# Kernel optimization log

Hardware: AMD Instinct MI355X
Metric: run time of the kernel (lower is better)

Reference implementation:

```python
import jax, jax.numpy as jnp
import numpy as np

TOP_K = 32
SCALE_FACTOR = 8.0
NEG_INF = -1e18


def setup_inputs() -> dict:
    key = jax.random.key(0)
    kq, kk, kv = jax.random.split(key, 3)
    B, H, S, D = 2, 16, 2048, 64
    q = jax.random.normal(kq, (B, H, S, D), dtype=jnp.float32)
    k = jax.random.normal(kk, (B, H, S, D), dtype=jnp.float32)
    v = jax.random.normal(kv, (B, H, S, D), dtype=jnp.float32)
    return {"q": q, "k": k, "v": v}


def reference(q, k, v):
    # scores: [B, H, Sq, Sk]
    scores = jnp.einsum("bhqd,bhkd->bhqk", q, k) / SCALE_FACTOR
    # torch code clamps top_k against key.size()[-1] == head dim D (quirk);
    # with TOP_K=32 < D=64 the clamp is inactive.
    top_k = min(TOP_K, k.shape[-1])
    topv, _ = jax.lax.top_k(scores, top_k)            # [B,H,Sq,top_k], sorted desc
    thresh = topv[..., -1:]                            # k-th largest per query row
    mask_k = scores < thresh                           # True -> masked out
    scores = jnp.where(mask_k, NEG_INF, scores)
    attn = jax.nn.softmax(scores, axis=-1)
    context = jnp.einsum("bhqk,bhkd->bhqd", attn, v)
    return context, attn, mask_k
```

## Files before the change

### kernel.cpp

```cpp
#include <hip/hip_runtime.h>
#include <math.h>

namespace {
constexpr int kS = 2048;
constexpr int kD = 64;
constexpr int kBH = 32;
constexpr int kTopK = 32;
constexpr int kBins = 4096;
constexpr int kMaxCand = 256;
constexpr int kKeepCap = 64;
constexpr size_t kCtxElems  = (size_t)kBH * kS * kD;
constexpr size_t kAttnElems = (size_t)kBH * kS * kS;
}

__device__ __forceinline__ unsigned sortable_bits(float x) {
  unsigned u = __float_as_uint(x);
  return u ^ ((u & 0x80000000u) ? 0xFFFFFFFFu : 0x80000000u);
}

__global__ __launch_bounds__(256) void qk_scores(const float* __restrict__ q,
                                                 const float* __restrict__ k,
                                                 float* __restrict__ scores) {
  __shared__ float QsT[64][132];
  __shared__ float KsT[64][132];
  const int bh  = blockIdx.z;
  const int q0  = blockIdx.y * 128;
  const int k0  = blockIdx.x * 128;
  const int tid = threadIdx.x;
  const float* qg = q + ((size_t)bh * kS + q0) * kD;
  const float* kg = k + ((size_t)bh * kS + k0) * kD;

#pragma unroll
  for (int rnd = 0; rnd < 8; ++rnd) {
    int flat = rnd * 1024 + tid * 4;
    int r = flat >> 6;
    int c = flat & 63;
    float4 qv = *(const float4*)(qg + flat);
    QsT[c + 0][r] = qv.x;
    QsT[c + 1][r] = qv.y;
    QsT[c + 2][r] = qv.z;
    QsT[c + 3][r] = qv.w;
    float4 kv = *(const float4*)(kg + flat);
    KsT[c + 0][r] = kv.x;
    KsT[c + 1][r] = kv.y;
    KsT[c + 2][r] = kv.z;
    KsT[c + 3][r] = kv.w;
  }
  __syncthreads();

  const int ty8 = (tid >> 4) * 8;
  const int tx8 = (tid & 15) * 8;
  float acc[8][8] = {};
#pragma unroll
  for (int kk = 0; kk < 64; kk += 4) {
    float a[4][8], b[4][8];
#pragma unroll
    for (int u = 0; u < 4; ++u) {
      *(float4*)(&a[u][0]) = *(const float4*)(&QsT[kk + u][ty8]);
      *(float4*)(&a[u][4]) = *(const float4*)(&QsT[kk + u][ty8 + 4]);
      *(float4*)(&b[u][0]) = *(const float4*)(&KsT[kk + u][tx8]);
      *(float4*)(&b[u][4]) = *(const float4*)(&KsT[kk + u][tx8 + 4]);
    }
#pragma unroll
    for (int i = 0; i < 8; ++i)
#pragma unroll
      for (int u = 0; u < 4; ++u)
#pragma unroll
        for (int j = 0; j < 8; ++j)
          acc[i][j] += a[u][i] * b[u][j];
  }

#pragma unroll
  for (int i = 0; i < 8; ++i) {
    float* orow = scores + ((size_t)bh * kS + q0 + ty8 + i) * kS + k0 + tx8;
    float4 o0 = make_float4(acc[i][0] * 0.125f, acc[i][1] * 0.125f,
                            acc[i][2] * 0.125f, acc[i][3] * 0.125f);
    float4 o1 = make_float4(acc[i][4] * 0.125f, acc[i][5] * 0.125f,
                            acc[i][6] * 0.125f, acc[i][7] * 0.125f);
    *(float4*)(orow)     = o0;
    *(float4*)(orow + 4) = o1;
  }
}

__global__ __launch_bounds__(256) void topk_softmax(const float* __restrict__ v,
                                                    float* __restrict__ ctx,
                                                    float* __restrict__ attn,
                                                    float* __restrict__ mask) {
  const int row  = blockIdx.x;
  const int bh   = row >> 11;
  const int tid  = threadIdx.x;
  const int lane = tid & 63;
  const int wid  = tid >> 6;

  __shared__ unsigned s_hist[kBins];
  __shared__ float    s_cand[kMaxCand];
  __shared__ int      s_kidx[kKeepCap];
  __shared__ float    s_kw[kKeepCap];
  __shared__ float    s_wmax[4], s_wsum[4];
  __shared__ unsigned s_T[4];
  __shared__ unsigned s_nc, s_nk;
  __shared__ int      s_bstar, s_gabove;
  __shared__ float    s_t32;

  const float* srow = attn + (size_t)row * kS;
  float4 l0 = *(const float4*)(srow + tid * 4);
  float4 l1 = *(const float4*)(srow + 1024 + tid * 4);
  float locv[8] = {l0.x, l0.y, l0.z, l0.w, l1.x, l1.y, l1.z, l1.w};
  int   loce[8];
#pragma unroll
  for (int j = 0; j < 8; ++j)
    loce[j] = (j < 4) ? (tid * 4 + j) : (1024 + tid * 4 + (j - 4));
#pragma unroll
  for (int i = 0; i < 4; ++i)
    *(uint4*)(&s_hist[tid * 16 + i * 4]) = make_uint4(0u, 0u, 0u, 0u);
  if (tid == 0) { s_nc = 0u; s_nk = 0u; }
  __syncthreads();

  unsigned bins[8];
  float pmax = locv[0];
#pragma unroll
  for (int j = 0; j < 8; ++j) {
    bins[j] = sortable_bits(locv[j]) >> 20;
    atomicAdd(&s_hist[bins[j]], 1u);
    pmax = fmaxf(pmax, locv[j]);
  }
#pragma unroll
  for (int off = 32; off >= 1; off >>= 1)
    pmax = fmaxf(pmax, __shfl_xor(pmax, off));
  if (lane == 0) s_wmax[wid] = pmax;
  __syncthreads();

  unsigned lsum = 0;
#pragma unroll
  for (int j = 0; j < 16; ++j) lsum += s_hist[tid * 16 + j];
  unsigned sfx = lsum;
#pragma unroll
  for (int off = 1; off < 64; off <<= 1) {
    unsigned z = __shfl_down(sfx, off);
    if (lane + off < 64) sfx += z;
  }
  if (lane == 0) s_T[wid] = sfx;
  __syncthreads();

  unsigned hi = 0;
#pragma unroll
  for (int w = 0; w < 4; ++w)
    if (w > wid) hi += s_T[w];
  unsigned gsfx  = sfx + hi;
  unsigned above = gsfx - lsum;
  if (gsfx >= (unsigned)kTopK && above < (unsigned)kTopK) {
    unsigned run = above;
    for (int j = 15; j >= 0; --j) {
      unsigned h = s_hist[tid * 16 + j];
      if (run < (unsigned)kTopK && run + h >= (unsigned)kTopK) {
        s_bstar  = tid * 16 + j;
        s_gabove = (int)run;
      }
      run += h;
    }
  }
  __syncthreads();
  const int   bstar  = s_bstar;
  const int   gabove = s_gabove;
  const float mx = fmaxf(fmaxf(s_wmax[0], s_wmax[1]),
                         fmaxf(s_wmax[2], s_wmax[3]));

#pragma unroll
  for (int j = 0; j < 8; ++j) {
    if ((int)bins[j] == bstar) {
      unsigned pos = atomicAdd(&s_nc, 1u);
      if (pos < (unsigned)kMaxCand) s_cand[pos] = locv[j];
    }
  }
  __syncthreads();
  const int m2 = (int)min(s_nc, (unsigned)kMaxCand);

  for (int c = tid; c < m2; c += 256) {
    float x = s_cand[c];
    int g = 0, e = 0;
    for (int j2 = 0; j2 < m2; ++j2) {
      float y = s_cand[j2];
      g += (y > x);
      e += (y == x);
    }
    int G = gabove + g;
    if (G < kTopK && G + e >= kTopK) s_t32 = x;
  }
  __syncthreads();
  const float t32 = s_t32;

  float w8[8];
  float psum = 0.0f;
#pragma unroll
  for (int j = 0; j < 8; ++j) {
    bool keep = (locv[j] >= t32);
    float wv = keep ? __expf(locv[j] - mx) : 0.0f;
    w8[j] = wv;
    psum += wv;
    if (keep) {
      unsigned p = atomicAdd(&s_nk, 1u);
      if (p < (unsigned)kKeepCap) { s_kidx[p] = loce[j]; s_kw[p] = wv; }
    }
  }
#pragma unroll
  for (int off = 32; off >= 1; off >>= 1)
    psum += __shfl_xor(psum, off);
  if (lane == 0) s_wsum[wid] = psum;
  __syncthreads();

  const float Z = s_wsum[0] + s_wsum[1] + s_wsum[2] + s_wsum[3];
  const float invZ = 1.0f / Z;

  float* arow = attn + (size_t)row * kS;
  float* mrow = mask + (size_t)row * kS;
  float4 a0 = make_float4(w8[0] * invZ, w8[1] * invZ, w8[2] * invZ, w8[3] * invZ);
  float4 a1 = make_float4(w8[4] * invZ, w8[5] * invZ, w8[6] * invZ, w8[7] * invZ);
  float4 m0 = make_float4(locv[0] >= t32 ? 0.f : 1.f, locv[1] >= t32 ? 0.f : 1.f,
                          locv[2] >= t32 ? 0.f : 1.f, locv[3] >= t32 ? 0.f : 1.f);
  float4 m1 = make_float4(locv[4] >= t32 ? 0.f : 1.f, locv[5] >= t32 ? 0.f : 1.f,
                          locv[6] >= t32 ? 0.f : 1.f, locv[7] >= t32 ? 0.f : 1.f);
  *(float4*)(arow + tid * 4)        = a0;
  *(float4*)(arow + 1024 + tid * 4) = a1;
  *(float4*)(mrow + tid * 4)        = m0;
  *(float4*)(mrow + 1024 + tid * 4) = m1;

  if (tid < kD) {
    const int nk = (int)min(s_nk, (unsigned)kKeepCap);
    float acc = 0.0f;
    for (int c = 0; c < nk; ++c)
      acc += s_kw[c] * v[((size_t)bh * kS + s_kidx[c]) * kD + tid];
    ctx[(size_t)row * kD + tid] = acc * invZ;
  }
}

extern "C" void kernel_launch(void* const* d_in, const int* in_sizes, int n_in,
                              void* d_out, int out_size, void* d_ws, size_t ws_size,
                              hipStream_t stream) {
  const float* q = (const float*)d_in[0];
  const float* k = (const float*)d_in[1];
  const float* v = (const float*)d_in[2];
  float* out  = (float*)d_out;
  float* ctx  = out;
  float* attn = out + kCtxElems;
  float* mask = attn + kAttnElems;

  dim3 g1(kS / 128, kS / 128, kBH);
  qk_scores<<<g1, 256, 0, stream>>>(q, k, attn);
  topk_softmax<<<dim3(kBH * kS), 256, 0, stream>>>(v, ctx, attn, mask);
}
```

Measured before the change: 1.434 ms.

## Process one top-k softmax row per wavefront and split QK staging into halves

```diff
diff --git a/kernel.cpp b/kernel.cpp
--- a/kernel.cpp
+++ b/kernel.cpp
@@ -6,8 +6,8 @@
 constexpr int kD = 64;
 constexpr int kBH = 32;
 constexpr int kTopK = 32;
-constexpr int kBins = 4096;
-constexpr int kMaxCand = 256;
+constexpr int kPadBins = 2112;
+constexpr int kCandCap = 128;
 constexpr int kKeepCap = 64;
 constexpr size_t kCtxElems  = (size_t)kBH * kS * kD;
 constexpr size_t kAttnElems = (size_t)kBH * kS * kS;
@@ -21,8 +21,8 @@
 __global__ __launch_bounds__(256) void qk_scores(const float* __restrict__ q,
                                                  const float* __restrict__ k,
                                                  float* __restrict__ scores) {
-  __shared__ float QsT[64][132];
-  __shared__ float KsT[64][132];
+  __shared__ float QsT[32][132];
+  __shared__ float KsT[32][132];
   const int bh  = blockIdx.z;
   const int q0  = blockIdx.y * 128;
   const int k0  = blockIdx.x * 128;
@@ -30,44 +30,43 @@
   const float* qg = q + ((size_t)bh * kS + q0) * kD;
   const float* kg = k + ((size_t)bh * kS + k0) * kD;
 
-#pragma unroll
-  for (int rnd = 0; rnd < 8; ++rnd) {
-    int flat = rnd * 1024 + tid * 4;
-    int r = flat >> 6;
-    int c = flat & 63;
-    float4 qv = *(const float4*)(qg + flat);
-    QsT[c + 0][r] = qv.x;
-    QsT[c + 1][r] = qv.y;
-    QsT[c + 2][r] = qv.z;
-    QsT[c + 3][r] = qv.w;
-    float4 kv = *(const float4*)(kg + flat);
-    KsT[c + 0][r] = kv.x;
-    KsT[c + 1][r] = kv.y;
-    KsT[c + 2][r] = kv.z;
-    KsT[c + 3][r] = kv.w;
-  }
-  __syncthreads();
-
   const int ty8 = (tid >> 4) * 8;
   const int tx8 = (tid & 15) * 8;
   float acc[8][8] = {};
-#pragma unroll
-  for (int kk = 0; kk < 64; kk += 4) {
-    float a[4][8], b[4][8];
-#pragma unroll
-    for (int u = 0; u < 4; ++u) {
-      *(float4*)(&a[u][0]) = *(const float4*)(&QsT[kk + u][ty8]);
-      *(float4*)(&a[u][4]) = *(const float4*)(&QsT[kk + u][ty8 + 4]);
-      *(float4*)(&b[u][0]) = *(const float4*)(&KsT[kk + u][tx8]);
-      *(float4*)(&b[u][4]) = *(const float4*)(&KsT[kk + u][tx8 + 4]);
-    }
-#pragma unroll
-    for (int i = 0; i < 8; ++i)
-#pragma unroll
-      for (int u = 0; u < 4; ++u)
+
+  for (int half = 0; half < 2; ++half) {
+    if (half) __syncthreads();
+#pragma unroll
+    for (int rnd = 0; rnd < 4; ++rnd) {
+      int flat = rnd * 1024 + tid * 4;
+      int r = flat >> 5;
+      int c = flat & 31;
+      float4 qv = *(const float4*)(qg + r * kD + half * 32 + c);
+      QsT[c + 0][r] = qv.x;
+      QsT[c + 1][r] = qv.y;
+      QsT[c + 2][r] = qv.z;
+      QsT[c + 3][r] = qv.w;
+      float4 kv = *(const float4*)(kg + r * kD + half * 32 + c);
+      KsT[c + 0][r] = kv.x;
+      KsT[c + 1][r] = kv.y;
+      KsT[c + 2][r] = kv.z;
+      KsT[c + 3][r] = kv.w;
+    }
+    __syncthreads();
+
+#pragma unroll
+    for (int kk = 0; kk < 32; ++kk) {
+      float a[8], b[8];
+      *(float4*)(&a[0]) = *(const float4*)(&QsT[kk][ty8]);
+      *(float4*)(&a[4]) = *(const float4*)(&QsT[kk][ty8 + 4]);
+      *(float4*)(&b[0]) = *(const float4*)(&KsT[kk][tx8]);
+      *(float4*)(&b[4]) = *(const float4*)(&KsT[kk][tx8 + 4]);
+#pragma unroll
+      for (int i = 0; i < 8; ++i)
 #pragma unroll
         for (int j = 0; j < 8; ++j)
-          acc[i][j] += a[u][i] * b[u][j];
+          acc[i][j] += a[i] * b[j];
+    }
   }
 
 #pragma unroll
@@ -86,151 +85,153 @@
                                                     float* __restrict__ ctx,
                                                     float* __restrict__ attn,
                                                     float* __restrict__ mask) {
-  const int row  = blockIdx.x;
+  __shared__ unsigned s_hist[4][kPadBins];
+  __shared__ float    s_cand[4][kCandCap];
+  __shared__ int      s_kidx[4][kKeepCap];
+  __shared__ float    s_kw[4][kKeepCap];
+  __shared__ unsigned s_nc[4], s_nk[4];
+
+  const int tid  = threadIdx.x;
+  const int wid  = tid >> 6;
+  const int lane = tid & 63;
+  const int row  = blockIdx.x * 4 + wid;
   const int bh   = row >> 11;
-  const int tid  = threadIdx.x;
-  const int lane = tid & 63;
-  const int wid  = tid >> 6;
-
-  __shared__ unsigned s_hist[kBins];
-  __shared__ float    s_cand[kMaxCand];
-  __shared__ int      s_kidx[kKeepCap];
-  __shared__ float    s_kw[kKeepCap];
-  __shared__ float    s_wmax[4], s_wsum[4];
-  __shared__ unsigned s_T[4];
-  __shared__ unsigned s_nc, s_nk;
-  __shared__ int      s_bstar, s_gabove;
-  __shared__ float    s_t32;
+  unsigned* hist = s_hist[wid];
 
   const float* srow = attn + (size_t)row * kS;
-  float4 l0 = *(const float4*)(srow + tid * 4);
-  float4 l1 = *(const float4*)(srow + 1024 + tid * 4);
-  float locv[8] = {l0.x, l0.y, l0.z, l0.w, l1.x, l1.y, l1.z, l1.w};
-  int   loce[8];
-#pragma unroll
-  for (int j = 0; j < 8; ++j)
-    loce[j] = (j < 4) ? (tid * 4 + j) : (1024 + tid * 4 + (j - 4));
-#pragma unroll
-  for (int i = 0; i < 4; ++i)
-    *(uint4*)(&s_hist[tid * 16 + i * 4]) = make_uint4(0u, 0u, 0u, 0u);
-  if (tid == 0) { s_nc = 0u; s_nk = 0u; }
-  __syncthreads();
-
-  unsigned bins[8];
+  float locv[32];
+#pragma unroll
+  for (int g = 0; g < 8; ++g)
+    *(float4*)(&locv[g * 4]) = *(const float4*)(srow + g * 256 + lane * 4);
+
+#pragma unroll
+  for (int j = 0; j < 33; ++j) hist[j * 64 + lane] = 0u;
+  if (lane == 0) { s_nc[wid] = 0u; s_nk[wid] = 0u; }
+
   float pmax = locv[0];
 #pragma unroll
-  for (int j = 0; j < 8; ++j) {
-    bins[j] = sortable_bits(locv[j]) >> 20;
-    atomicAdd(&s_hist[bins[j]], 1u);
+  for (int j = 0; j < 32; ++j) {
+    unsigned b = sortable_bits(locv[j]) >> 21;
+    atomicAdd(&hist[b + (b >> 5)], 1u);
     pmax = fmaxf(pmax, locv[j]);
   }
 #pragma unroll
   for (int off = 32; off >= 1; off >>= 1)
     pmax = fmaxf(pmax, __shfl_xor(pmax, off));
-  if (lane == 0) s_wmax[wid] = pmax;
-  __syncthreads();
+
+  asm volatile("s_waitcnt lgkmcnt(0)" ::: "memory");
 
   unsigned lsum = 0;
 #pragma unroll
-  for (int j = 0; j < 16; ++j) lsum += s_hist[tid * 16 + j];
+  for (int j = 0; j < 32; ++j) lsum += hist[lane * 33 + j];
   unsigned sfx = lsum;
 #pragma unroll
   for (int off = 1; off < 64; off <<= 1) {
     unsigned z = __shfl_down(sfx, off);
     if (lane + off < 64) sfx += z;
   }
-  if (lane == 0) s_T[wid] = sfx;
-  __syncthreads();
-
-  unsigned hi = 0;
-#pragma unroll
-  for (int w = 0; w < 4; ++w)
-    if (w > wid) hi += s_T[w];
-  unsigned gsfx  = sfx + hi;
-  unsigned above = gsfx - lsum;
-  if (gsfx >= (unsigned)kTopK && above < (unsigned)kTopK) {
+  const unsigned above = sfx - lsum;
+
+  int bstar = 0, gabove = 0;
+  const bool ispiv = (sfx >= (unsigned)kTopK) && (above < (unsigned)kTopK);
+  if (ispiv) {
     unsigned run = above;
-    for (int j = 15; j >= 0; --j) {
-      unsigned h = s_hist[tid * 16 + j];
+    for (int j = 31; j >= 0; --j) {
+      unsigned h = hist[lane * 33 + j];
       if (run < (unsigned)kTopK && run + h >= (unsigned)kTopK) {
-        s_bstar  = tid * 16 + j;
-        s_gabove = (int)run;
+        bstar  = lane * 32 + j;
+        gabove = (int)run;
       }
       run += h;
     }
   }
-  __syncthreads();
-  const int   bstar  = s_bstar;
-  const int   gabove = s_gabove;
-  const float mx = fmaxf(fmaxf(s_wmax[0], s_wmax[1]),
-                         fmaxf(s_wmax[2], s_wmax[3]));
-
-#pragma unroll
-  for (int j = 0; j < 8; ++j) {
-    if ((int)bins[j] == bstar) {
-      unsigned pos = atomicAdd(&s_nc, 1u);
-      if (pos < (unsigned)kMaxCand) s_cand[pos] = locv[j];
-    }
-  }
-  __syncthreads();
-  const int m2 = (int)min(s_nc, (unsigned)kMaxCand);
-
-  for (int c = tid; c < m2; c += 256) {
-    float x = s_cand[c];
-    int g = 0, e = 0;
-    for (int j2 = 0; j2 < m2; ++j2) {
-      float y = s_cand[j2];
-      g += (y > x);
-      e += (y == x);
-    }
-    int G = gabove + g;
-    if (G < kTopK && G + e >= kTopK) s_t32 = x;
-  }
-  __syncthreads();
-  const float t32 = s_t32;
-
-  float w8[8];
+  const unsigned long long pm = __ballot(ispiv);
+  const int psrc = __ffsll(pm) - 1;
+  bstar  = __shfl(bstar, psrc);
+  gabove = __shfl(gabove, psrc);
+
+#pragma unroll
+  for (int j = 0; j < 32; ++j) {
+    unsigned b = sortable_bits(locv[j]) >> 21;
+    if ((int)b == bstar) {
+      unsigned p = atomicAdd(&s_nc[wid], 1u);
+      if (p < (unsigned)kCandCap) s_cand[wid][p] = locv[j];
+    }
+  }
+  asm volatile("s_waitcnt lgkmcnt(0)" ::: "memory");
+  const int m = (int)min(s_nc[wid], (unsigned)kCandCap);
+
+  const float x0 = (lane < m) ? s_cand[wid][lane] : 0.0f;
+  const float x1 = (lane + 64 < m) ? s_cand[wid][lane + 64] : 0.0f;
+  int g0 = 0, e0 = 0, g1 = 0, e1 = 0;
+  for (int j = 0; j < m; ++j) {
+    float y = s_cand[wid][j];
+    g0 += (y > x0); e0 += (y == x0);
+    g1 += (y > x1); e1 += (y == x1);
+  }
+  const bool win0 = (lane < m) &&
+                    (gabove + g0 < kTopK) && (gabove + g0 + e0 >= kTopK);
+  const bool win1 = (lane + 64 < m) &&
+                    (gabove + g1 < kTopK) && (gabove + g1 + e1 >= kTopK);
+  const unsigned long long wm0 = __ballot(win0);
+  const unsigned long long wm1 = __ballot(win1);
+  float t32;
+  if (wm0 != 0ull)      t32 = __shfl(x0, __ffsll(wm0) - 1);
+  else if (wm1 != 0ull) t32 = __shfl(x1, __ffsll(wm1) - 1);
+  else                  t32 = pmax;
+
+  float w32[32];
   float psum = 0.0f;
 #pragma unroll
-  for (int j = 0; j < 8; ++j) {
-    bool keep = (locv[j] >= t32);
-    float wv = keep ? __expf(locv[j] - mx) : 0.0f;
-    w8[j] = wv;
+  for (int j = 0; j < 32; ++j) {
+    const bool keep = (locv[j] >= t32);
+    const float wv = keep ? __expf(locv[j] - pmax) : 0.0f;
+    w32[j] = wv;
     psum += wv;
     if (keep) {
-      unsigned p = atomicAdd(&s_nk, 1u);
-      if (p < (unsigned)kKeepCap) { s_kidx[p] = loce[j]; s_kw[p] = wv; }
+      unsigned p = atomicAdd(&s_nk[wid], 1u);
+      if (p < (unsigned)kKeepCap) {
+        s_kidx[wid][p] = (j >> 2) * 256 + lane * 4 + (j & 3);
+        s_kw[wid][p]   = wv;
+      }
     }
   }
 #pragma unroll
   for (int off = 32; off >= 1; off >>= 1)
     psum += __shfl_xor(psum, off);
-  if (lane == 0) s_wsum[wid] = psum;
-  __syncthreads();
-
-  const float Z = s_wsum[0] + s_wsum[1] + s_wsum[2] + s_wsum[3];
-  const float invZ = 1.0f / Z;
+  const float invZ = 1.0f / psum;
 
   float* arow = attn + (size_t)row * kS;
   float* mrow = mask + (size_t)row * kS;
-  float4 a0 = make_float4(w8[0] * invZ, w8[1] * invZ, w8[2] * invZ, w8[3] * invZ);
-  float4 a1 = make_float4(w8[4] * invZ, w8[5] * invZ, w8[6] * invZ, w8[7] * invZ);
-  float4 m0 = make_float4(locv[0] >= t32 ? 0.f : 1.f, locv[1] >= t32 ? 0.f : 1.f,
-                          locv[2] >= t32 ? 0.f : 1.f, locv[3] >= t32 ? 0.f : 1.f);
-  float4 m1 = make_float4(locv[4] >= t32 ? 0.f : 1.f, locv[5] >= t32 ? 0.f : 1.f,
-                          locv[6] >= t32 ? 0.f : 1.f, locv[7] >= t32 ? 0.f : 1.f);
-  *(float4*)(arow + tid * 4)        = a0;
-  *(float4*)(arow + 1024 + tid * 4) = a1;
-  *(float4*)(mrow + tid * 4)        = m0;
-  *(float4*)(mrow + 1024 + tid * 4) = m1;
-
-  if (tid < kD) {
-    const int nk = (int)min(s_nk, (unsigned)kKeepCap);
-    float acc = 0.0f;
-    for (int c = 0; c < nk; ++c)
-      acc += s_kw[c] * v[((size_t)bh * kS + s_kidx[c]) * kD + tid];
-    ctx[(size_t)row * kD + tid] = acc * invZ;
-  }
+#pragma unroll
+  for (int g = 0; g < 8; ++g) {
+    float4 a = make_float4(w32[g*4+0] * invZ, w32[g*4+1] * invZ,
+                           w32[g*4+2] * invZ, w32[g*4+3] * invZ);
+    float4 mm = make_float4(locv[g*4+0] >= t32 ? 0.f : 1.f,
+                            locv[g*4+1] >= t32 ? 0.f : 1.f,
+                            locv[g*4+2] >= t32 ? 0.f : 1.f,
+                            locv[g*4+3] >= t32 ? 0.f : 1.f);
+    *(float4*)(arow + g * 256 + lane * 4) = a;
+    *(float4*)(mrow + g * 256 + lane * 4) = mm;
+  }
+
+  asm volatile("s_waitcnt lgkmcnt(0)" ::: "memory");
+  const int nk = (int)min(s_nk[wid], (unsigned)kKeepCap);
+  const float* vb = v + ((size_t)bh * kS) * kD + lane;
+  float acc = 0.0f;
+  int c = 0;
+  for (; c + 4 <= nk; c += 4) {
+    const float w0 = s_kw[wid][c+0], w1 = s_kw[wid][c+1];
+    const float w2 = s_kw[wid][c+2], w3 = s_kw[wid][c+3];
+    const int   i0 = s_kidx[wid][c+0], i1 = s_kidx[wid][c+1];
+    const int   i2 = s_kidx[wid][c+2], i3 = s_kidx[wid][c+3];
+    const float v0 = vb[(size_t)i0 * kD], v1 = vb[(size_t)i1 * kD];
+    const float v2 = vb[(size_t)i2 * kD], v3 = vb[(size_t)i3 * kD];
+    acc += w0 * v0; acc += w1 * v1; acc += w2 * v2; acc += w3 * v3;
+  }
+  for (; c < nk; ++c)
+    acc += s_kw[wid][c] * vb[(size_t)s_kidx[wid][c] * kD];
+  ctx[(size_t)row * kD + lane] = acc * invZ;
 }
 
 extern "C" void kernel_launch(void* const* d_in, const int* in_sizes, int n_in,
@@ -246,5 +247,5 @@
 
   dim3 g1(kS / 128, kS / 128, kBH);
   qk_scores<<<g1, 256, 0, stream>>>(q, k, attn);
-  topk_softmax<<<dim3(kBH * kS), 256, 0, stream>>>(v, ctx, attn, mask);
-}
+  topk_softmax<<<dim3(kBH * kS / 4), 256, 0, stream>>>(v, ctx, attn, mask);
+}
```

Result: no change. 1.428 ms (-0.4%).
